# Kernel tuning notes

Measured on AMD Instinct MI355X. Metric: run time of the kernel, lower is better.

The kernel has to match this reference:

```python
import jax, jax.numpy as jnp
import numpy as np

B, S, E = 2, 2048, 2048
H = 16
KV_RANK = 512
ROPE = 64
NOPE = 64  # source sets qk_nope_dim = qk_rope_dim
VD = 128   # v_head_dim = head_dim
QD = ROPE + NOPE  # q_head_dim = 128


def setup_inputs() -> dict:
    key = jax.random.key(0)
    ks = jax.random.split(key, 5)
    sd = lambda fan_in: 1.0 / np.sqrt(fan_in)
    return {
        "x": jax.random.normal(ks[0], (B, S, E), jnp.float32),
        "attention_mask": jnp.zeros((1, 1, S, S), jnp.float32),
        "W_kv_down": jax.random.normal(ks[1], (KV_RANK + ROPE, E), jnp.float32) * sd(E),
        "W_kv_up": jax.random.normal(ks[2], (H * (VD + NOPE), KV_RANK), jnp.float32) * sd(KV_RANK),
        "W_q": jax.random.normal(ks[3], (H * QD, E), jnp.float32) * sd(E),
        "W_out": jax.random.normal(ks[4], (E, H * VD), jnp.float32) * sd(H * VD),
    }


def reference(x, attention_mask, W_kv_down, W_kv_up, W_q, W_out):
    scale = QD ** (-0.5)
    # down-project to latent + rope part
    compressed = jnp.einsum('bse,fe->bsf', x, W_kv_down)          # [B,S,KV_RANK+ROPE]
    kv_c, k_rope = compressed[..., :KV_RANK], compressed[..., KV_RANK:]
    # up-project latent to per-head v and k_nope
    kv_exp = jnp.einsum('bsr,fr->bsf', kv_c, W_kv_up)             # [B,S,H*(VD+NOPE)]
    kv_exp = kv_exp.reshape(B, S, H, VD + NOPE).transpose(0, 2, 1, 3)  # [B,H,S,VD+NOPE]
    v, k_nope = kv_exp[..., :VD], kv_exp[..., VD:]
    # shared rope key broadcast over heads, concat [rope, nope]
    k_rope_b = jnp.broadcast_to(k_rope[:, None], (B, H, S, ROPE))
    k = jnp.concatenate([k_rope_b, k_nope], axis=-1)              # [B,H,S,QD]
    # queries
    q = jnp.einsum('bse,fe->bsf', x, W_q).reshape(B, S, H, QD).transpose(0, 2, 1, 3)
    scores = jnp.einsum('bhsd,bhtd->bhst', q, k) * scale + attention_mask
    w = jax.nn.softmax(scores, axis=-1)
    out = jnp.einsum('bhst,bhtv->bhsv', w, v)                     # [B,H,S,VD]
    out = out.transpose(0, 2, 1, 3).reshape(B, S, H * VD)
    return jnp.einsum('bsf,ef->bse', out, W_out)
```

## Files before the change

kernel.cpp:

```cpp
#include <hip/hip_runtime.h>
#include <hip/hip_bf16.h>
#include <stdint.h>

typedef __bf16 bf16x8 __attribute__((ext_vector_type(8)));
typedef float f32x4 __attribute__((ext_vector_type(4)));
typedef float f32x16 __attribute__((ext_vector_type(16)));
typedef uint32_t u32x4 __attribute__((ext_vector_type(4)));
typedef unsigned short ushort_t;
typedef unsigned short ushort8v __attribute__((ext_vector_type(8)));

#define MFMA16 __builtin_amdgcn_mfma_f32_16x16x32_bf16
#define MFMA32 __builtin_amdgcn_mfma_f32_32x32x16_bf16

static constexpr int Bc = 2, Sc = 2048, Ec = 2048, Hc = 16;

__device__ __forceinline__ void gload16(const void* g, void* l) {
  __builtin_amdgcn_global_load_lds(
      (const __attribute__((address_space(1))) void*)g,
      (__attribute__((address_space(3))) void*)l, 16, 0, 0);
}

__device__ __forceinline__ ushort_t f2bf(float f) {
  uint32_t u = __float_as_uint(f);
  uint32_t r = (u + 0x7fffu + ((u >> 16) & 1u)) >> 16;
  return (ushort_t)r;
}
__device__ __forceinline__ float bf2f(ushort_t u) {
  return __uint_as_float((uint32_t)u << 16);
}
__device__ __forceinline__ uint32_t cvtpk(float a, float b) {
  uint32_t d;
  asm("v_cvt_pk_bf16_f32 %0, %1, %2" : "=v"(d) : "v"(a), "v"(b));
  return d;
}
__device__ __forceinline__ void plswap(uint32_t& a, uint32_t& b) {
  asm("v_permlane32_swap_b32 %0, %1" : "+v"(a), "+v"(b));
}

__global__ void cast_all(const float* __restrict__ x, const float* __restrict__ Wq,
                         const float* __restrict__ Wkvu, const float* __restrict__ Wout,
                         const float* __restrict__ Wkvd,
                         ushort_t* __restrict__ xb, ushort_t* __restrict__ wq,
                         ushort_t* __restrict__ wkvu, ushort_t* __restrict__ wout,
                         ushort_t* __restrict__ wkvd) {
  int i = blockIdx.x * 256 + threadIdx.x;
  const float* src;
  ushort_t* dst;
  int j;
  if (i < 2097152) { src = x; dst = xb; j = i; }
  else if (i < 3145728) { src = Wq; dst = wq; j = i - 2097152; }
  else if (i < 3538944) { src = Wkvu; dst = wkvu; j = i - 3145728; }
  else if (i < 4587520) { src = Wout; dst = wout; j = i - 3538944; }
  else {
    j = i - 4587520;
    int row = j >> 9, col4 = j & 511;
    ushort4 o;
    if (row < 576) {
      float4 v = ((const float4*)Wkvd)[row * 512 + col4];
      o.x = f2bf(v.x); o.y = f2bf(v.y); o.z = f2bf(v.z); o.w = f2bf(v.w);
    } else { o.x = 0; o.y = 0; o.z = 0; o.w = 0; }
    ((ushort4*)wkvd)[j] = o;
    return;
  }
  float4 v = ((const float4*)src)[j];
  ushort4 o;
  o.x = f2bf(v.x); o.y = f2bf(v.y); o.z = f2bf(v.z); o.w = f2bf(v.w);
  ((ushort4*)dst)[j] = o;
}

__global__ void mask_rearrange(const float* __restrict__ mask, ushort_t* __restrict__ m4) {
  const float INVLN2 = 1.4426950408889634f;
  int i = blockIdx.x * 256 + threadIdx.x;
  if (i >= 524288) return;
  int rr = i & 1, half = (i >> 1) & 1, kblk = (i >> 2) & 1, kt = (i >> 3) & 31, q = i >> 8;
  const float* src = mask + (size_t)q * 2048 + kt * 64 + kblk * 32 + half * 4 + rr * 16;
  float4 a = *(const float4*)src;
  float4 c = *(const float4*)(src + 8);
  ushort8v o;
  o[0] = f2bf(a.x * INVLN2); o[1] = f2bf(a.y * INVLN2);
  o[2] = f2bf(a.z * INVLN2); o[3] = f2bf(a.w * INVLN2);
  o[4] = f2bf(c.x * INVLN2); o[5] = f2bf(c.y * INVLN2);
  o[6] = f2bf(c.z * INVLN2); o[7] = f2bf(c.w * INVLN2);
  ((ushort8v*)m4)[i] = o;
}

template<int MODE>
__global__ __launch_bounds__(256, 2)
void gemm_bt(const ushort_t* __restrict__ A, int lda,
             const ushort_t* __restrict__ Bm, int ldb,
             void* __restrict__ Cout, int ldc,
             int M, int N, int K,
             char* __restrict__ vtb, char* __restrict__ kbuf)
{
  __shared__ __align__(16) ushort_t sA[2][128 * 32];
  __shared__ __align__(16) ushort_t sB[2][128 * 32];
  int tid = threadIdx.x;
  int nTn = N >> 7;
  int bid = blockIdx.x;
  int chunk = gridDim.x >> 3;
  bid = (bid & 7) * chunk + (bid >> 3);
  int tm = bid / nTn, tn = bid - tm * nTn;
  int wave = tid >> 6, lane = tid & 63;
  int wm = (wave >> 1) << 6, wn = (wave & 1) << 6;
  int l16 = lane & 15, g16 = lane >> 4;
  f32x4 acc[4][4] = {};
  int srow = tid >> 2, scol = (tid & 3) << 3;
  const ushort_t* Ag = A + (size_t)(tm * 128 + srow) * lda + scol;
  const ushort_t* Bg = Bm + (size_t)(tn * 128 + srow) * ldb + scol;
  ushort_t* sA0 = &sA[0][srow * 32 + scol];
  ushort_t* sA1 = &sA[1][srow * 32 + scol];
  ushort_t* sB0 = &sB[0][srow * 32 + scol];
  ushort_t* sB1 = &sB[1][srow * 32 + scol];
  for (int kt = 0; kt < K; kt += 64) {
    gload16(Ag, sA0);
    gload16(Ag + (size_t)64 * lda, sA0 + 64 * 32);
    gload16(Ag + 32, sA1);
    gload16(Ag + (size_t)64 * lda + 32, sA1 + 64 * 32);
    gload16(Bg, sB0);
    gload16(Bg + (size_t)64 * ldb, sB0 + 64 * 32);
    gload16(Bg + 32, sB1);
    gload16(Bg + (size_t)64 * ldb + 32, sB1 + 64 * 32);
    Ag += 64; Bg += 64;
    __syncthreads();
#pragma unroll
    for (int h2 = 0; h2 < 2; h2++) {
      bf16x8 af[4], bfr[4];
#pragma unroll
      for (int i = 0; i < 4; i++) af[i] = *(const bf16x8*)&sA[h2][(wm + i * 16 + l16) * 32 + g16 * 8];
#pragma unroll
      for (int i = 0; i < 4; i++) bfr[i] = *(const bf16x8*)&sB[h2][(wn + i * 16 + l16) * 32 + g16 * 8];
#pragma unroll
      for (int i = 0; i < 4; i++)
#pragma unroll
        for (int j = 0; j < 4; j++)
          acc[i][j] = MFMA16(af[i], bfr[j], acc[i][j], 0, 0, 0);
    }
    __syncthreads();
  }
#pragma unroll
  for (int i = 0; i < 4; i++) {
#pragma unroll
    for (int j = 0; j < 4; j++) {
      int grow0 = tm * 128 + wm + i * 16 + g16 * 4;
      int gcol = tn * 128 + wn + j * 16 + l16;
      if constexpr (MODE == 0) {
#pragma unroll
        for (int r = 0; r < 4; r++)
          ((ushort_t*)Cout)[(size_t)(grow0 + r) * ldc + gcol] = f2bf(acc[i][j][r]);
      } else if constexpr (MODE == 2) {
#pragma unroll
        for (int r = 0; r < 4; r++)
          ((float*)Cout)[(size_t)(grow0 + r) * ldc + gcol] = acc[i][j][r];
      } else {
        int h = gcol / 192, jj = gcol - h * 192;
        int b = grow0 >> 11, s0 = grow0 & 2047;
        size_t bh = (size_t)(b * Hc + h);
        if (jj < 128) {
          ushort4 pk;
          pk.x = f2bf(acc[i][j][0]); pk.y = f2bf(acc[i][j][1]);
          pk.z = f2bf(acc[i][j][2]); pk.w = f2bf(acc[i][j][3]);
          *(ushort4*)(vtb + bh * 524288 + (size_t)jj * 4096 + ((s0 >> 6) * 128) +
                      ((2 * (s0 & 63)) ^ ((jj & 7) << 4))) = pk;
        } else {
          int col = 64 + (jj - 128);
#pragma unroll
          for (int r = 0; r < 4; r++) {
            int s = s0 + r;
            *(ushort_t*)(kbuf + (bh * Sc + s) * 256 + ((2 * col) ^ ((s & 7) << 4))) = f2bf(acc[i][j][r]);
          }
        }
      }
    }
  }
}

__global__ void rope_fill(const ushort_t* __restrict__ comp, char* __restrict__ kbuf) {
  int i = blockIdx.x * 256 + threadIdx.x;
  if (i >= Bc * Sc * 8) return;
  int blk = i & 7;
  int m = i >> 3;
  int s = m & 2047, b = m >> 11;
  uint4 v = *(const uint4*)&comp[(size_t)m * 640 + 512 + blk * 8];
  int off = (blk * 16) ^ ((s & 7) << 4);
#pragma unroll
  for (int h = 0; h < Hc; h++) {
    *(uint4*)(kbuf + ((size_t)(b * Hc + h) * Sc + s) * 256 + off) = v;
  }
}

__global__ __launch_bounds__(128, 2)
void attn_kernel(const ushort_t* __restrict__ qb, const char* __restrict__ kbuf,
                 const char* __restrict__ vtb, const ushort_t* __restrict__ m4,
                 ushort_t* __restrict__ attn_o)
{
  __shared__ __align__(16) char smem[32768];
  char* sK = smem;
  char* sV = smem + 16384;
  const float scale2 = 0.12752081738040466f;
  int bid = blockIdx.x;
  bid = (bid & 7) * 128 + (bid >> 3);
  int qt = bid & 31, bh = bid >> 5;
  int b = bh >> 4, h = bh & 15;
  int tid = threadIdx.x, wave = tid >> 6, lane = tid & 63;
  int l32 = lane & 31, half = lane >> 5;
  int sx = (l32 & 7) << 4;
  int qbase = qt * 64 + wave * 32;

  bf16x8 qf[8];
  {
    const ushort_t* qp = qb + (size_t)(b * Sc + qbase + l32) * 2048 + h * 128 + half * 8;
#pragma unroll
    for (int ks = 0; ks < 8; ks++) qf[ks] = *(const bf16x8*)(qp + ks * 16);
  }

  float mrun = -3.0e38f, lrun = 0.f;
  f32x16 acco[4] = {};

  const char* kg = kbuf + (size_t)bh * 524288;
  const char* vg = vtb + (size_t)bh * 524288;
  const ushort8v* mq = (const ushort8v*)m4 + (size_t)(qbase + l32) * 256 + half * 2;

  for (int kt = 0; kt < 32; kt++) {
#pragma unroll
    for (int it = 0; it < 8; it++)
      gload16(kg + kt * 16384 + it * 2048 + tid * 16, sK + it * 2048 + tid * 16);
#pragma unroll
    for (int it = 0; it < 8; it++) {
      int l = it * 2048 + tid * 16;
      gload16(vg + (size_t)(l >> 7) * 4096 + kt * 128 + (l & 127), sV + l);
    }
    ushort8v mvv[4];
#pragma unroll
    for (int kb = 0; kb < 2; kb++)
#pragma unroll
      for (int rr = 0; rr < 2; rr++)
        mvv[kb * 2 + rr] = mq[kt * 8 + kb * 4 + rr];
    __syncthreads();

#pragma unroll
    for (int kblk = 0; kblk < 2; kblk++) {
      f32x16 sc = {};
      __builtin_amdgcn_s_setprio(1);
#pragma unroll
      for (int ks = 0; ks < 8; ks++) {
        bf16x8 kfr = *(const bf16x8*)(sK + (kblk * 32 + l32) * 256 +
                                      ((ks * 32 + half * 16) ^ sx));
        sc = MFMA32(kfr, qf[ks], sc, 0, 0, 0);
      }
      __builtin_amdgcn_s_setprio(0);

#pragma unroll
      for (int r = 0; r < 16; r++)
        sc[r] = sc[r] * scale2 + bf2f(mvv[kblk * 2 + (r >> 3)][r & 7]);
      float mx = sc[0];
#pragma unroll
      for (int r = 1; r < 16; r++) mx = fmaxf(mx, sc[r]);
      mx = fmaxf(mx, __shfl_xor(mx, 32));
      if (!__all(mx <= mrun + 11.0f)) {
        float mnew = fmaxf(mrun, mx);
        float corr = __builtin_amdgcn_exp2f(mrun - mnew);
        lrun *= corr; mrun = mnew;
#pragma unroll
        for (int r = 0; r < 16; r++) {
          float cr = __shfl(corr, (r & 3) + 8 * (r >> 2) + 4 * half);
#pragma unroll
          for (int vb = 0; vb < 4; vb++) acco[vb][r] *= cr;
        }
      }
      float rs = 0.f;
      uint32_t W[8];
#pragma unroll
      for (int m = 0; m < 4; m++) {
        float p0 = __builtin_amdgcn_exp2f(sc[4 * m + 0] - mrun);
        float p1 = __builtin_amdgcn_exp2f(sc[4 * m + 1] - mrun);
        float p2 = __builtin_amdgcn_exp2f(sc[4 * m + 2] - mrun);
        float p3 = __builtin_amdgcn_exp2f(sc[4 * m + 3] - mrun);
        rs += (p0 + p1) + (p2 + p3);
        W[2 * m] = cvtpk(p0, p1);
        W[2 * m + 1] = cvtpk(p2, p3);
      }
      lrun += rs;

      bf16x8 pf[2];
#pragma unroll
      for (int k2 = 0; k2 < 2; k2++) {
        uint32_t a0 = W[4 * k2 + 0], a1 = W[4 * k2 + 1];
        uint32_t b0 = W[4 * k2 + 2], b1 = W[4 * k2 + 3];
        plswap(a0, b0);
        plswap(a1, b1);
        u32x4 t; t[0] = a0; t[1] = a1; t[2] = b0; t[3] = b1;
        pf[k2] = __builtin_bit_cast(bf16x8, t);
      }

      __builtin_amdgcn_s_setprio(1);
#pragma unroll
      for (int k2 = 0; k2 < 2; k2++)
#pragma unroll
        for (int vb = 0; vb < 4; vb++) {
          bf16x8 vf = *(const bf16x8*)(sV + (vb * 32 + l32) * 128 +
                                       ((kblk * 64 + k2 * 32 + half * 16) ^ sx));
          acco[vb] = MFMA32(pf[k2], vf, acco[vb], 0, 0, 0);
        }
      __builtin_amdgcn_s_setprio(0);
    }

    __syncthreads();
  }

  lrun += __shfl_xor(lrun, 32);
#pragma unroll
  for (int r = 0; r < 16; r++) {
    int rowq = (r & 3) + 8 * (r >> 2) + 4 * half;
    float lr = __shfl(lrun, rowq);
    float inv = 1.0f / lr;
    int qrow = qbase + rowq;
    ushort_t* op = attn_o + (size_t)(b * Sc + qrow) * 2048 + h * 128 + l32;
#pragma unroll
    for (int vb = 0; vb < 4; vb++)
      op[vb * 32] = f2bf(acco[vb][r] * inv);
  }
}

extern "C" void kernel_launch(void* const* d_in, const int* in_sizes, int n_in,
                              void* d_out, int out_size, void* d_ws, size_t ws_size,
                              hipStream_t stream) {
  const float* x    = (const float*)d_in[0];
  const float* mask = (const float*)d_in[1];
  const float* Wkvd = (const float*)d_in[2];
  const float* Wkvu = (const float*)d_in[3];
  const float* Wq   = (const float*)d_in[4];
  const float* Wout = (const float*)d_in[5];

  char* ws = (char*)d_ws;
  size_t off = 0;
  auto alloc = [&](size_t bytes) { char* p = ws + off; off += (bytes + 255) & ~(size_t)255; return p; };
  ushort_t* xb   = (ushort_t*)alloc((size_t)4096 * 2048 * 2);
  ushort_t* wkvd = (ushort_t*)alloc((size_t)640 * 2048 * 2);
  ushort_t* wq   = (ushort_t*)alloc((size_t)2048 * 2048 * 2);
  ushort_t* wkvu = (ushort_t*)alloc((size_t)3072 * 512 * 2);
  ushort_t* wout = (ushort_t*)alloc((size_t)2048 * 2048 * 2);
  ushort_t* comp = (ushort_t*)alloc((size_t)4096 * 640 * 2);
  ushort_t* qbuf = (ushort_t*)alloc((size_t)4096 * 2048 * 2);
  char*     kbuf = alloc((size_t)Bc * Hc * Sc * 256);
  char*     vtb  = alloc((size_t)Bc * Hc * 524288);
  ushort_t* attn_o = xb;
  ushort_t* m4 = wq;

  cast_all<<<19200, 256, 0, stream>>>(x, Wq, Wkvu, Wout, Wkvd, xb, wq, wkvu, wout, wkvd);

  gemm_bt<0><<<32 * 5, 256, 0, stream>>>(xb, 2048, wkvd, 2048, comp, 640, 4096, 640, 2048, nullptr, nullptr);
  gemm_bt<0><<<32 * 16, 256, 0, stream>>>(xb, 2048, wq, 2048, qbuf, 2048, 4096, 2048, 2048, nullptr, nullptr);
  mask_rearrange<<<2048, 256, 0, stream>>>(mask, m4);
  gemm_bt<1><<<32 * 24, 256, 0, stream>>>(comp, 640, wkvu, 512, nullptr, 0, 4096, 3072, 512, vtb, kbuf);
  rope_fill<<<32768 / 256, 256, 0, stream>>>(comp, kbuf);
  attn_kernel<<<1024, 128, 0, stream>>>(qbuf, kbuf, vtb, m4, attn_o);
  gemm_bt<2><<<32 * 16, 256, 0, stream>>>(attn_o, 2048, wout, 2048, d_out, 2048, 4096, 2048, 2048, nullptr, nullptr);
}
```

Measured before the change: 263.0 us.

## Double-buffer GEMM LDS tiles and prefetch next K-slice during MFMA

Restructures the GEMM main loop to use two LDS buffers per K-half, issuing async global-to-LDS loads for the next K tile while computing on the current one, with vmcnt-based waits and raw barriers instead of full syncthreads. It also raises wave priority around the MFMA block. This aims to hide global load latency behind matrix math. In exchange it doubles LDS use to 64KB per block, which may reduce occupancy below the two blocks per CU the launch bounds request. The last iteration issues a redundant reload of tile zero.

```diff
diff --git a/kernel.cpp b/kernel.cpp
--- a/kernel.cpp
+++ b/kernel.cpp
@@ -92,8 +92,8 @@
              int M, int N, int K,
              char* __restrict__ vtb, char* __restrict__ kbuf)
 {
-  __shared__ __align__(16) ushort_t sA[2][128 * 32];
-  __shared__ __align__(16) ushort_t sB[2][128 * 32];
+  __shared__ __align__(16) ushort_t sA[2][2][128 * 32];
+  __shared__ __align__(16) ushort_t sB[2][2][128 * 32];
   int tid = threadIdx.x;
   int nTn = N >> 7;
   int bid = blockIdx.x;
@@ -107,36 +107,48 @@
   int srow = tid >> 2, scol = (tid & 3) << 3;
   const ushort_t* Ag = A + (size_t)(tm * 128 + srow) * lda + scol;
   const ushort_t* Bg = Bm + (size_t)(tn * 128 + srow) * ldb + scol;
-  ushort_t* sA0 = &sA[0][srow * 32 + scol];
-  ushort_t* sA1 = &sA[1][srow * 32 + scol];
-  ushort_t* sB0 = &sB[0][srow * 32 + scol];
-  ushort_t* sB1 = &sB[1][srow * 32 + scol];
-  for (int kt = 0; kt < K; kt += 64) {
-    gload16(Ag, sA0);
-    gload16(Ag + (size_t)64 * lda, sA0 + 64 * 32);
-    gload16(Ag + 32, sA1);
-    gload16(Ag + (size_t)64 * lda + 32, sA1 + 64 * 32);
-    gload16(Bg, sB0);
-    gload16(Bg + (size_t)64 * ldb, sB0 + 64 * 32);
-    gload16(Bg + 32, sB1);
-    gload16(Bg + (size_t)64 * ldb + 32, sB1 + 64 * 32);
-    Ag += 64; Bg += 64;
-    __syncthreads();
-#pragma unroll
-    for (int h2 = 0; h2 < 2; h2++) {
+  int Kt = K >> 6;
+
+  auto ISSUE = [&](int kk, int nb, int ks) {
+    const ushort_t* As = Ag + kk + ks * 32;
+    const ushort_t* Bs = Bg + kk + ks * 32;
+    ushort_t* dA = &sA[nb][ks][srow * 32 + scol];
+    ushort_t* dB = &sB[nb][ks][srow * 32 + scol];
+    gload16(As, dA);
+    gload16(As + (size_t)64 * lda, dA + 64 * 32);
+    gload16(Bs, dB);
+    gload16(Bs + (size_t)64 * ldb, dB + 64 * 32);
+  };
+
+  ISSUE(0, 0, 0);
+  ISSUE(0, 0, 1);
+  asm volatile("s_waitcnt vmcnt(4)" ::: "memory");
+  __builtin_amdgcn_s_barrier();
+
+  for (int kt = 0; kt < Kt; kt++) {
+    int buf = kt & 1;
+    int nb = (kt + 1) & 1;
+    int kkn = ((kt + 1) == Kt) ? 0 : (kt + 1) * 64;
+#pragma unroll
+    for (int ks = 0; ks < 2; ks++) {
+      ISSUE(kkn, nb, ks);
       bf16x8 af[4], bfr[4];
 #pragma unroll
-      for (int i = 0; i < 4; i++) af[i] = *(const bf16x8*)&sA[h2][(wm + i * 16 + l16) * 32 + g16 * 8];
-#pragma unroll
-      for (int i = 0; i < 4; i++) bfr[i] = *(const bf16x8*)&sB[h2][(wn + i * 16 + l16) * 32 + g16 * 8];
+      for (int i = 0; i < 4; i++) af[i] = *(const bf16x8*)&sA[buf][ks][(wm + i * 16 + l16) * 32 + g16 * 8];
+#pragma unroll
+      for (int i = 0; i < 4; i++) bfr[i] = *(const bf16x8*)&sB[buf][ks][(wn + i * 16 + l16) * 32 + g16 * 8];
+      __builtin_amdgcn_s_setprio(1);
 #pragma unroll
       for (int i = 0; i < 4; i++)
 #pragma unroll
         for (int j = 0; j < 4; j++)
           acc[i][j] = MFMA16(af[i], bfr[j], acc[i][j], 0, 0, 0);
+      __builtin_amdgcn_s_setprio(0);
+      asm volatile("s_waitcnt vmcnt(4)" ::: "memory");
+      __builtin_amdgcn_s_barrier();
     }
-    __syncthreads();
-  }
+  }
+
 #pragma unroll
   for (int i = 0; i < 4; i++) {
 #pragma unroll
```

After: 290.9 us. 10.6% more time.

## Software-pipeline K/V tile loads in attention and merge mask/rope prep kernels

Applied to the files above, without the earlier changes.

The attention inner loop is restructured so the next K tile is issued right after the QK MFMAs and the next V tile right after the PV MFMAs. Explicit vmcnt waits and barriers replace the full __syncthreads pair, so global-to-LDS copies overlap with the softmax and matmul work. Both 32-key sub-blocks are now computed together with a single max/rescale per 64-key tile, and the mask prefetch is double-buffered. Separately, the mask rearrange and rope fill kernels are merged into one launch to save a kernel launch. This relies on hand-counted vmcnt values and on single-buffered LDS reuse being correct, and it raises register pressure.

```diff
diff --git a/kernel.cpp b/kernel.cpp
--- a/kernel.cpp
+++ b/kernel.cpp
@@ -68,20 +68,34 @@
   ((ushort4*)dst)[j] = o;
 }
 
-__global__ void mask_rearrange(const float* __restrict__ mask, ushort_t* __restrict__ m4) {
+__global__ void prep_kernel(const float* __restrict__ mask, ushort_t* __restrict__ m4,
+                            const ushort_t* __restrict__ comp, char* __restrict__ kbuf) {
   const float INVLN2 = 1.4426950408889634f;
-  int i = blockIdx.x * 256 + threadIdx.x;
-  if (i >= 524288) return;
-  int rr = i & 1, half = (i >> 1) & 1, kblk = (i >> 2) & 1, kt = (i >> 3) & 31, q = i >> 8;
-  const float* src = mask + (size_t)q * 2048 + kt * 64 + kblk * 32 + half * 4 + rr * 16;
-  float4 a = *(const float4*)src;
-  float4 c = *(const float4*)(src + 8);
-  ushort8v o;
-  o[0] = f2bf(a.x * INVLN2); o[1] = f2bf(a.y * INVLN2);
-  o[2] = f2bf(a.z * INVLN2); o[3] = f2bf(a.w * INVLN2);
-  o[4] = f2bf(c.x * INVLN2); o[5] = f2bf(c.y * INVLN2);
-  o[6] = f2bf(c.z * INVLN2); o[7] = f2bf(c.w * INVLN2);
-  ((ushort8v*)m4)[i] = o;
+  int gb = blockIdx.x;
+  if (gb < 2048) {
+    int i = gb * 256 + threadIdx.x;
+    int rr = i & 1, half = (i >> 1) & 1, kblk = (i >> 2) & 1, kt = (i >> 3) & 31, q = i >> 8;
+    const float* src = mask + (size_t)q * 2048 + kt * 64 + kblk * 32 + half * 4 + rr * 16;
+    float4 a = *(const float4*)src;
+    float4 c = *(const float4*)(src + 8);
+    ushort8v o;
+    o[0] = f2bf(a.x * INVLN2); o[1] = f2bf(a.y * INVLN2);
+    o[2] = f2bf(a.z * INVLN2); o[3] = f2bf(a.w * INVLN2);
+    o[4] = f2bf(c.x * INVLN2); o[5] = f2bf(c.y * INVLN2);
+    o[6] = f2bf(c.z * INVLN2); o[7] = f2bf(c.w * INVLN2);
+    ((ushort8v*)m4)[i] = o;
+  } else {
+    int i = (gb - 2048) * 256 + threadIdx.x;
+    int blk = i & 7;
+    int m = i >> 3;
+    int s = m & 2047, b = m >> 11;
+    uint4 v = *(const uint4*)&comp[(size_t)m * 640 + 512 + blk * 8];
+    int off = (blk * 16) ^ ((s & 7) << 4);
+#pragma unroll
+    for (int h = 0; h < Hc; h++) {
+      *(uint4*)(kbuf + ((size_t)(b * Hc + h) * Sc + s) * 256 + off) = v;
+    }
+  }
 }
 
 template<int MODE>
@@ -174,20 +188,6 @@
   }
 }
 
-__global__ void rope_fill(const ushort_t* __restrict__ comp, char* __restrict__ kbuf) {
-  int i = blockIdx.x * 256 + threadIdx.x;
-  if (i >= Bc * Sc * 8) return;
-  int blk = i & 7;
-  int m = i >> 3;
-  int s = m & 2047, b = m >> 11;
-  uint4 v = *(const uint4*)&comp[(size_t)m * 640 + 512 + blk * 8];
-  int off = (blk * 16) ^ ((s & 7) << 4);
-#pragma unroll
-  for (int h = 0; h < Hc; h++) {
-    *(uint4*)(kbuf + ((size_t)(b * Hc + h) * Sc + s) * 256 + off) = v;
-  }
-}
-
 __global__ __launch_bounds__(128, 2)
 void attn_kernel(const ushort_t* __restrict__ qb, const char* __restrict__ kbuf,
                  const char* __restrict__ vtb, const ushort_t* __restrict__ m4,
@@ -220,91 +220,130 @@
   const char* vg = vtb + (size_t)bh * 524288;
   const ushort8v* mq = (const ushort8v*)m4 + (size_t)(qbase + l32) * 256 + half * 2;
 
-  for (int kt = 0; kt < 32; kt++) {
+  auto ISSUE_K = [&](int kt) {
 #pragma unroll
     for (int it = 0; it < 8; it++)
       gload16(kg + kt * 16384 + it * 2048 + tid * 16, sK + it * 2048 + tid * 16);
+  };
+  auto ISSUE_V = [&](int kt) {
 #pragma unroll
     for (int it = 0; it < 8; it++) {
       int l = it * 2048 + tid * 16;
       gload16(vg + (size_t)(l >> 7) * 4096 + kt * 128 + (l & 127), sV + l);
     }
-    ushort8v mvv[4];
-#pragma unroll
-    for (int kb = 0; kb < 2; kb++)
-#pragma unroll
-      for (int rr = 0; rr < 2; rr++)
-        mvv[kb * 2 + rr] = mq[kt * 8 + kb * 4 + rr];
-    __syncthreads();
-
-#pragma unroll
-    for (int kblk = 0; kblk < 2; kblk++) {
-      f32x16 sc = {};
-      __builtin_amdgcn_s_setprio(1);
-#pragma unroll
-      for (int ks = 0; ks < 8; ks++) {
-        bf16x8 kfr = *(const bf16x8*)(sK + (kblk * 32 + l32) * 256 +
-                                      ((ks * 32 + half * 16) ^ sx));
-        sc = MFMA32(kfr, qf[ks], sc, 0, 0, 0);
-      }
-      __builtin_amdgcn_s_setprio(0);
-
-#pragma unroll
-      for (int r = 0; r < 16; r++)
-        sc[r] = sc[r] * scale2 + bf2f(mvv[kblk * 2 + (r >> 3)][r & 7]);
-      float mx = sc[0];
-#pragma unroll
-      for (int r = 1; r < 16; r++) mx = fmaxf(mx, sc[r]);
-      mx = fmaxf(mx, __shfl_xor(mx, 32));
-      if (!__all(mx <= mrun + 11.0f)) {
-        float mnew = fmaxf(mrun, mx);
-        float corr = __builtin_amdgcn_exp2f(mrun - mnew);
-        lrun *= corr; mrun = mnew;
-#pragma unroll
-        for (int r = 0; r < 16; r++) {
-          float cr = __shfl(corr, (r & 3) + 8 * (r >> 2) + 4 * half);
-#pragma unroll
-          for (int vb = 0; vb < 4; vb++) acco[vb][r] *= cr;
-        }
-      }
-      float rs = 0.f;
-      uint32_t W[8];
-#pragma unroll
-      for (int m = 0; m < 4; m++) {
-        float p0 = __builtin_amdgcn_exp2f(sc[4 * m + 0] - mrun);
-        float p1 = __builtin_amdgcn_exp2f(sc[4 * m + 1] - mrun);
-        float p2 = __builtin_amdgcn_exp2f(sc[4 * m + 2] - mrun);
-        float p3 = __builtin_amdgcn_exp2f(sc[4 * m + 3] - mrun);
-        rs += (p0 + p1) + (p2 + p3);
-        W[2 * m] = cvtpk(p0, p1);
-        W[2 * m + 1] = cvtpk(p2, p3);
-      }
-      lrun += rs;
-
-      bf16x8 pf[2];
-#pragma unroll
-      for (int k2 = 0; k2 < 2; k2++) {
-        uint32_t a0 = W[4 * k2 + 0], a1 = W[4 * k2 + 1];
-        uint32_t b0 = W[4 * k2 + 2], b1 = W[4 * k2 + 3];
-        plswap(a0, b0);
-        plswap(a1, b1);
+  };
+
+  auto TILE = [&](int kt, ushort8v (&mc)[4], ushort8v (&mn)[4]) {
+    int ktn = (kt + 1) & 31;
+    asm volatile("s_waitcnt vmcnt(8)" ::: "memory");
+    __builtin_amdgcn_s_barrier();
+
+    f32x16 sc0 = {}, sc1 = {};
+    __builtin_amdgcn_s_setprio(1);
+#pragma unroll
+    for (int ks = 0; ks < 8; ks++) {
+      bf16x8 k0 = *(const bf16x8*)(sK + l32 * 256 + ((ks * 32 + half * 16) ^ sx));
+      bf16x8 k1 = *(const bf16x8*)(sK + (32 + l32) * 256 + ((ks * 32 + half * 16) ^ sx));
+      sc0 = MFMA32(k0, qf[ks], sc0, 0, 0, 0);
+      sc1 = MFMA32(k1, qf[ks], sc1, 0, 0, 0);
+    }
+    __builtin_amdgcn_s_setprio(0);
+    __builtin_amdgcn_s_barrier();
+
+    mn[0] = mq[ktn * 8 + 0]; mn[1] = mq[ktn * 8 + 1];
+    mn[2] = mq[ktn * 8 + 4]; mn[3] = mq[ktn * 8 + 5];
+    ISSUE_K(ktn);
+
+#pragma unroll
+    for (int r = 0; r < 16; r++) {
+      sc0[r] = sc0[r] * scale2 + bf2f(mc[r >> 3][r & 7]);
+      sc1[r] = sc1[r] * scale2 + bf2f(mc[2 + (r >> 3)][r & 7]);
+    }
+    float mx = fmaxf(sc0[0], sc1[0]);
+#pragma unroll
+    for (int r = 1; r < 16; r++) mx = fmaxf(mx, fmaxf(sc0[r], sc1[r]));
+    mx = fmaxf(mx, __shfl_xor(mx, 32));
+    if (!__all(mx <= mrun + 11.0f)) {
+      float mnew = fmaxf(mrun, mx);
+      float corr = __builtin_amdgcn_exp2f(mrun - mnew);
+      lrun *= corr; mrun = mnew;
+#pragma unroll
+      for (int r = 0; r < 16; r++) {
+        float cr = __shfl(corr, (r & 3) + 8 * (r >> 2) + 4 * half);
+#pragma unroll
+        for (int vb = 0; vb < 4; vb++) acco[vb][r] *= cr;
+      }
+    }
+    float rs = 0.f;
+    uint32_t W0[8], W1[8];
+#pragma unroll
+    for (int m = 0; m < 4; m++) {
+      float a0 = __builtin_amdgcn_exp2f(sc0[4 * m + 0] - mrun);
+      float a1 = __builtin_amdgcn_exp2f(sc0[4 * m + 1] - mrun);
+      float a2 = __builtin_amdgcn_exp2f(sc0[4 * m + 2] - mrun);
+      float a3 = __builtin_amdgcn_exp2f(sc0[4 * m + 3] - mrun);
+      float b0 = __builtin_amdgcn_exp2f(sc1[4 * m + 0] - mrun);
+      float b1 = __builtin_amdgcn_exp2f(sc1[4 * m + 1] - mrun);
+      float b2 = __builtin_amdgcn_exp2f(sc1[4 * m + 2] - mrun);
+      float b3 = __builtin_amdgcn_exp2f(sc1[4 * m + 3] - mrun);
+      rs += (a0 + a1) + (a2 + a3) + (b0 + b1) + (b2 + b3);
+      W0[2 * m] = cvtpk(a0, a1); W0[2 * m + 1] = cvtpk(a2, a3);
+      W1[2 * m] = cvtpk(b0, b1); W1[2 * m + 1] = cvtpk(b2, b3);
+    }
+    lrun += rs;
+
+    bf16x8 pf0[2], pf1[2];
+#pragma unroll
+    for (int k2 = 0; k2 < 2; k2++) {
+      {
+        uint32_t a0 = W0[4 * k2 + 0], a1 = W0[4 * k2 + 1];
+        uint32_t b0 = W0[4 * k2 + 2], b1 = W0[4 * k2 + 3];
+        plswap(a0, b0); plswap(a1, b1);
         u32x4 t; t[0] = a0; t[1] = a1; t[2] = b0; t[3] = b1;
-        pf[k2] = __builtin_bit_cast(bf16x8, t);
-      }
-
-      __builtin_amdgcn_s_setprio(1);
-#pragma unroll
-      for (int k2 = 0; k2 < 2; k2++)
-#pragma unroll
-        for (int vb = 0; vb < 4; vb++) {
-          bf16x8 vf = *(const bf16x8*)(sV + (vb * 32 + l32) * 128 +
-                                       ((kblk * 64 + k2 * 32 + half * 16) ^ sx));
-          acco[vb] = MFMA32(pf[k2], vf, acco[vb], 0, 0, 0);
-        }
-      __builtin_amdgcn_s_setprio(0);
-    }
-
-    __syncthreads();
+        pf0[k2] = __builtin_bit_cast(bf16x8, t);
+      }
+      {
+        uint32_t a0 = W1[4 * k2 + 0], a1 = W1[4 * k2 + 1];
+        uint32_t b0 = W1[4 * k2 + 2], b1 = W1[4 * k2 + 3];
+        plswap(a0, b0); plswap(a1, b1);
+        u32x4 t; t[0] = a0; t[1] = a1; t[2] = b0; t[3] = b1;
+        pf1[k2] = __builtin_bit_cast(bf16x8, t);
+      }
+    }
+
+    asm volatile("s_waitcnt vmcnt(12)" ::: "memory");
+    __builtin_amdgcn_s_barrier();
+
+    __builtin_amdgcn_s_setprio(1);
+#pragma unroll
+    for (int k2 = 0; k2 < 2; k2++) {
+#pragma unroll
+      for (int vb = 0; vb < 4; vb++) {
+        bf16x8 vf = *(const bf16x8*)(sV + (vb * 32 + l32) * 128 +
+                                     ((k2 * 32 + half * 16) ^ sx));
+        acco[vb] = MFMA32(pf0[k2], vf, acco[vb], 0, 0, 0);
+      }
+#pragma unroll
+      for (int vb = 0; vb < 4; vb++) {
+        bf16x8 vf = *(const bf16x8*)(sV + (vb * 32 + l32) * 128 +
+                                     ((64 + k2 * 32 + half * 16) ^ sx));
+        acco[vb] = MFMA32(pf1[k2], vf, acco[vb], 0, 0, 0);
+      }
+    }
+    __builtin_amdgcn_s_setprio(0);
+    __builtin_amdgcn_s_barrier();
+    ISSUE_V(ktn);
+  };
+
+  ushort8v mcA[4], mcB[4];
+  mcA[0] = mq[0]; mcA[1] = mq[1]; mcA[2] = mq[4]; mcA[3] = mq[5];
+  ISSUE_K(0);
+  ISSUE_V(0);
+
+#pragma unroll 1
+  for (int kt = 0; kt < 32; kt += 2) {
+    TILE(kt, mcA, mcB);
+    TILE(kt + 1, mcB, mcA);
   }
 
   lrun += __shfl_xor(lrun, 32);
@@ -350,9 +389,8 @@
 
   gemm_bt<0><<<32 * 5, 256, 0, stream>>>(xb, 2048, wkvd, 2048, comp, 640, 4096, 640, 2048, nullptr, nullptr);
   gemm_bt<0><<<32 * 16, 256, 0, stream>>>(xb, 2048, wq, 2048, qbuf, 2048, 4096, 2048, 2048, nullptr, nullptr);
-  mask_rearrange<<<2048, 256, 0, stream>>>(mask, m4);
+  prep_kernel<<<2176, 256, 0, stream>>>(mask, m4, comp, kbuf);
   gemm_bt<1><<<32 * 24, 256, 0, stream>>>(comp, 640, wkvu, 512, nullptr, 0, 4096, 3072, 512, vtb, kbuf);
-  rope_fill<<<32768 / 256, 256, 0, stream>>>(comp, kbuf);
   attn_kernel<<<1024, 128, 0, stream>>>(qbuf, kbuf, vtb, m4, attn_o);
   gemm_bt<2><<<32 * 16, 256, 0, stream>>>(attn_o, 2048, wout, 2048, d_out, 2048, 4096, 2048, 2048, nullptr, nullptr);
 }
```

Measured after the change: 264.6 us. No clear change (+0.6%).

## Load attention K/V fragments directly to registers via fragment-ordered layouts

Applied to the files above, without the earlier changes.

The attention kernel now runs as single-wave blocks that read K and V straight from global memory into MFMA-ready register fragments, with the next K block register-prefetched. This removes the LDS staging and the __syncthreads barriers. To make those loads coalesced, the KV up-projection epilogue, the rope fill and the mask rearrangement now write K, V^T and the mask in fragment order. The rope fill is also merged into the mask-prep kernel, saving a launch. In exchange, each wave re-reads K/V from global/L2 with no sharing between waves, and register pressure rises.

```diff
diff --git a/kernel.cpp b/kernel.cpp
--- a/kernel.cpp
+++ b/kernel.cpp
@@ -68,20 +68,37 @@
   ((ushort4*)dst)[j] = o;
 }
 
-__global__ void mask_rearrange(const float* __restrict__ mask, ushort_t* __restrict__ m4) {
+__global__ void prep_kernel(const float* __restrict__ mask, ushort_t* __restrict__ m4,
+                            const ushort_t* __restrict__ comp, char* __restrict__ kbuf) {
   const float INVLN2 = 1.4426950408889634f;
-  int i = blockIdx.x * 256 + threadIdx.x;
-  if (i >= 524288) return;
-  int rr = i & 1, half = (i >> 1) & 1, kblk = (i >> 2) & 1, kt = (i >> 3) & 31, q = i >> 8;
-  const float* src = mask + (size_t)q * 2048 + kt * 64 + kblk * 32 + half * 4 + rr * 16;
-  float4 a = *(const float4*)src;
-  float4 c = *(const float4*)(src + 8);
-  ushort8v o;
-  o[0] = f2bf(a.x * INVLN2); o[1] = f2bf(a.y * INVLN2);
-  o[2] = f2bf(a.z * INVLN2); o[3] = f2bf(a.w * INVLN2);
-  o[4] = f2bf(c.x * INVLN2); o[5] = f2bf(c.y * INVLN2);
-  o[6] = f2bf(c.z * INVLN2); o[7] = f2bf(c.w * INVLN2);
-  ((ushort8v*)m4)[i] = o;
+  int gb = blockIdx.x;
+  if (gb < 2048) {
+    int i = gb * 256 + threadIdx.x;
+    int rr = i & 1, half = (i >> 1) & 1, kblk = (i >> 2) & 1, kt = (i >> 3) & 31, q = i >> 8;
+    const float* src = mask + (size_t)q * 2048 + kt * 64 + kblk * 32 + half * 4 + rr * 16;
+    float4 a = *(const float4*)src;
+    float4 c = *(const float4*)(src + 8);
+    ushort8v o;
+    o[0] = f2bf(a.x * INVLN2); o[1] = f2bf(a.y * INVLN2);
+    o[2] = f2bf(a.z * INVLN2); o[3] = f2bf(a.w * INVLN2);
+    o[4] = f2bf(c.x * INVLN2); o[5] = f2bf(c.y * INVLN2);
+    o[6] = f2bf(c.z * INVLN2); o[7] = f2bf(c.w * INVLN2);
+    size_t u5 = ((((size_t)(q >> 5) * 32 + kt) * 4 + kblk * 2 + rr) * 64) + half * 32 + (q & 31);
+    ((ushort8v*)m4)[u5] = o;
+  } else {
+    int i = (gb - 2048) * 256 + threadIdx.x;
+    int blk = i & 7;
+    int m = i >> 3;
+    int s = m & 2047, b = m >> 11;
+    uint4 v = *(const uint4*)&comp[(size_t)m * 640 + 512 + blk * 8];
+    int kt = s >> 6, kblk = (s & 63) >> 5;
+    size_t base = (size_t)kt * 16384 + kblk * 8192 + (blk >> 1) * 1024 +
+                  ((blk & 1) * 32 + (s & 31)) * 16;
+#pragma unroll
+    for (int h = 0; h < Hc; h++) {
+      *(uint4*)(kbuf + (size_t)(b * Hc + h) * 524288 + base) = v;
+    }
+  }
 }
 
 template<int MODE>
@@ -155,56 +172,41 @@
         int h = gcol / 192, jj = gcol - h * 192;
         int b = grow0 >> 11, s0 = grow0 & 2047;
         size_t bh = (size_t)(b * Hc + h);
+        int kt = s0 >> 6, sl = s0 & 63;
+        int kblk = sl >> 5, l32s = sl & 31;
         if (jj < 128) {
+          int k2 = (sl >> 4) & 1, halfv = (sl >> 3) & 1, e0 = sl & 7;
           ushort4 pk;
           pk.x = f2bf(acc[i][j][0]); pk.y = f2bf(acc[i][j][1]);
           pk.z = f2bf(acc[i][j][2]); pk.w = f2bf(acc[i][j][3]);
-          *(ushort4*)(vtb + bh * 524288 + (size_t)jj * 4096 + ((s0 >> 6) * 128) +
-                      ((2 * (s0 & 63)) ^ ((jj & 7) << 4))) = pk;
+          *(ushort4*)(vtb + bh * 524288 + (size_t)kt * 16384 + kblk * 8192 + k2 * 4096 +
+                      (jj >> 5) * 1024 + (halfv * 32 + (jj & 31)) * 16 + e0 * 2) = pk;
         } else {
-          int col = 64 + (jj - 128);
-#pragma unroll
-          for (int r = 0; r < 4; r++) {
-            int s = s0 + r;
-            *(ushort_t*)(kbuf + (bh * Sc + s) * 256 + ((2 * col) ^ ((s & 7) << 4))) = f2bf(acc[i][j][r]);
-          }
+          int qd = jj - 64;
+          int ks = qd >> 4, halfq = (qd >> 3) & 1, e = qd & 7;
+          char* kp = kbuf + bh * 524288 + (size_t)kt * 16384 + kblk * 8192 + ks * 1024 +
+                     (halfq * 32 + l32s) * 16 + e * 2;
+#pragma unroll
+          for (int r = 0; r < 4; r++)
+            *(ushort_t*)(kp + r * 16) = f2bf(acc[i][j][r]);
         }
       }
     }
   }
 }
 
-__global__ void rope_fill(const ushort_t* __restrict__ comp, char* __restrict__ kbuf) {
-  int i = blockIdx.x * 256 + threadIdx.x;
-  if (i >= Bc * Sc * 8) return;
-  int blk = i & 7;
-  int m = i >> 3;
-  int s = m & 2047, b = m >> 11;
-  uint4 v = *(const uint4*)&comp[(size_t)m * 640 + 512 + blk * 8];
-  int off = (blk * 16) ^ ((s & 7) << 4);
-#pragma unroll
-  for (int h = 0; h < Hc; h++) {
-    *(uint4*)(kbuf + ((size_t)(b * Hc + h) * Sc + s) * 256 + off) = v;
-  }
-}
-
-__global__ __launch_bounds__(128, 2)
+__global__ __launch_bounds__(64, 2)
 void attn_kernel(const ushort_t* __restrict__ qb, const char* __restrict__ kbuf,
                  const char* __restrict__ vtb, const ushort_t* __restrict__ m4,
                  ushort_t* __restrict__ attn_o)
 {
-  __shared__ __align__(16) char smem[32768];
-  char* sK = smem;
-  char* sV = smem + 16384;
   const float scale2 = 0.12752081738040466f;
   int bid = blockIdx.x;
-  bid = (bid & 7) * 128 + (bid >> 3);
-  int qt = bid & 31, bh = bid >> 5;
+  bid = (bid & 7) * 256 + (bid >> 3);
+  int qt = bid & 63, bh = bid >> 6;
   int b = bh >> 4, h = bh & 15;
-  int tid = threadIdx.x, wave = tid >> 6, lane = tid & 63;
-  int l32 = lane & 31, half = lane >> 5;
-  int sx = (l32 & 7) << 4;
-  int qbase = qt * 64 + wave * 32;
+  int l = threadIdx.x, l32 = l & 31, half = l >> 5;
+  int qbase = qt * 32;
 
   bf16x8 qf[8];
   {
@@ -218,93 +220,95 @@
 
   const char* kg = kbuf + (size_t)bh * 524288;
   const char* vg = vtb + (size_t)bh * 524288;
-  const ushort8v* mq = (const ushort8v*)m4 + (size_t)(qbase + l32) * 256 + half * 2;
-
+  const ushort8v* mbase = (const ushort8v*)m4 + (size_t)qt * 8192;
+  int moff = half * 32 + l32;
+
+  bf16x8 kfA[8], kfB[8];
+  {
+    const char* p = kg + l * 16;
+#pragma unroll
+    for (int ks = 0; ks < 8; ks++) kfA[ks] = *(const bf16x8*)(p + ks * 1024);
+  }
+
+  auto PHASE = [&](int kt, int kblk, bf16x8 (&kfc)[8], bf16x8 (&kfn)[8],
+                   int ktn, int nkblk) {
+    bf16x8 vv[8];
+    {
+      const char* p = vg + (size_t)kt * 16384 + kblk * 8192 + l * 16;
+#pragma unroll
+      for (int i2 = 0; i2 < 8; i2++) vv[i2] = *(const bf16x8*)(p + i2 * 1024);
+    }
+    ushort8v mca = mbase[(kt * 4 + kblk * 2) * 64 + moff];
+    ushort8v mcb = mbase[(kt * 4 + kblk * 2 + 1) * 64 + moff];
+
+    f32x16 sc = {};
+    __builtin_amdgcn_s_setprio(1);
+#pragma unroll
+    for (int ks = 0; ks < 8; ks++) sc = MFMA32(kfc[ks], qf[ks], sc, 0, 0, 0);
+    __builtin_amdgcn_s_setprio(0);
+
+    {
+      const char* p = kg + (size_t)ktn * 16384 + nkblk * 8192 + l * 16;
+#pragma unroll
+      for (int ks = 0; ks < 8; ks++) kfn[ks] = *(const bf16x8*)(p + ks * 1024);
+    }
+
+#pragma unroll
+    for (int r = 0; r < 16; r++)
+      sc[r] = sc[r] * scale2 + bf2f((r < 8 ? mca : mcb)[r & 7]);
+    float mx = sc[0];
+#pragma unroll
+    for (int r = 1; r < 16; r++) mx = fmaxf(mx, sc[r]);
+    mx = fmaxf(mx, __shfl_xor(mx, 32));
+    if (!__all(mx <= mrun + 11.0f)) {
+      float mnew = fmaxf(mrun, mx);
+      float corr = __builtin_amdgcn_exp2f(mrun - mnew);
+      lrun *= corr; mrun = mnew;
+#pragma unroll
+      for (int r = 0; r < 16; r++) {
+        float cr = __shfl(corr, (r & 3) + 8 * (r >> 2) + 4 * half);
+#pragma unroll
+        for (int vb = 0; vb < 4; vb++) acco[vb][r] *= cr;
+      }
+    }
+    float rs = 0.f;
+    uint32_t W[8];
+#pragma unroll
+    for (int m = 0; m < 4; m++) {
+      float p0 = __builtin_amdgcn_exp2f(sc[4 * m + 0] - mrun);
+      float p1 = __builtin_amdgcn_exp2f(sc[4 * m + 1] - mrun);
+      float p2 = __builtin_amdgcn_exp2f(sc[4 * m + 2] - mrun);
+      float p3 = __builtin_amdgcn_exp2f(sc[4 * m + 3] - mrun);
+      rs += (p0 + p1) + (p2 + p3);
+      W[2 * m] = cvtpk(p0, p1);
+      W[2 * m + 1] = cvtpk(p2, p3);
+    }
+    lrun += rs;
+
+    bf16x8 pf[2];
+#pragma unroll
+    for (int k2 = 0; k2 < 2; k2++) {
+      uint32_t a0 = W[4 * k2 + 0], a1 = W[4 * k2 + 1];
+      uint32_t b0 = W[4 * k2 + 2], b1 = W[4 * k2 + 3];
+      plswap(a0, b0);
+      plswap(a1, b1);
+      u32x4 t; t[0] = a0; t[1] = a1; t[2] = b0; t[3] = b1;
+      pf[k2] = __builtin_bit_cast(bf16x8, t);
+    }
+
+    __builtin_amdgcn_s_setprio(1);
+#pragma unroll
+    for (int k2 = 0; k2 < 2; k2++)
+#pragma unroll
+      for (int vb = 0; vb < 4; vb++)
+        acco[vb] = MFMA32(pf[k2], vv[k2 * 4 + vb], acco[vb], 0, 0, 0);
+    __builtin_amdgcn_s_setprio(0);
+  };
+
+#pragma unroll 1
   for (int kt = 0; kt < 32; kt++) {
-#pragma unroll
-    for (int it = 0; it < 8; it++)
-      gload16(kg + kt * 16384 + it * 2048 + tid * 16, sK + it * 2048 + tid * 16);
-#pragma unroll
-    for (int it = 0; it < 8; it++) {
-      int l = it * 2048 + tid * 16;
-      gload16(vg + (size_t)(l >> 7) * 4096 + kt * 128 + (l & 127), sV + l);
-    }
-    ushort8v mvv[4];
-#pragma unroll
-    for (int kb = 0; kb < 2; kb++)
-#pragma unroll
-      for (int rr = 0; rr < 2; rr++)
-        mvv[kb * 2 + rr] = mq[kt * 8 + kb * 4 + rr];
-    __syncthreads();
-
-#pragma unroll
-    for (int kblk = 0; kblk < 2; kblk++) {
-      f32x16 sc = {};
-      __builtin_amdgcn_s_setprio(1);
-#pragma unroll
-      for (int ks = 0; ks < 8; ks++) {
-        bf16x8 kfr = *(const bf16x8*)(sK + (kblk * 32 + l32) * 256 +
-                                      ((ks * 32 + half * 16) ^ sx));
-        sc = MFMA32(kfr, qf[ks], sc, 0, 0, 0);
-      }
-      __builtin_amdgcn_s_setprio(0);
-
-#pragma unroll
-      for (int r = 0; r < 16; r++)
-        sc[r] = sc[r] * scale2 + bf2f(mvv[kblk * 2 + (r >> 3)][r & 7]);
-      float mx = sc[0];
-#pragma unroll
-      for (int r = 1; r < 16; r++) mx = fmaxf(mx, sc[r]);
-      mx = fmaxf(mx, __shfl_xor(mx, 32));
-      if (!__all(mx <= mrun + 11.0f)) {
-        float mnew = fmaxf(mrun, mx);
-        float corr = __builtin_amdgcn_exp2f(mrun - mnew);
-        lrun *= corr; mrun = mnew;
-#pragma unroll
-        for (int r = 0; r < 16; r++) {
-          float cr = __shfl(corr, (r & 3) + 8 * (r >> 2) + 4 * half);
-#pragma unroll
-          for (int vb = 0; vb < 4; vb++) acco[vb][r] *= cr;
-        }
-      }
-      float rs = 0.f;
-      uint32_t W[8];
-#pragma unroll
-      for (int m = 0; m < 4; m++) {
-        float p0 = __builtin_amdgcn_exp2f(sc[4 * m + 0] - mrun);
-        float p1 = __builtin_amdgcn_exp2f(sc[4 * m + 1] - mrun);
-        float p2 = __builtin_amdgcn_exp2f(sc[4 * m + 2] - mrun);
-        float p3 = __builtin_amdgcn_exp2f(sc[4 * m + 3] - mrun);
-        rs += (p0 + p1) + (p2 + p3);
-        W[2 * m] = cvtpk(p0, p1);
-        W[2 * m + 1] = cvtpk(p2, p3);
-      }
-      lrun += rs;
-
-      bf16x8 pf[2];
-#pragma unroll
-      for (int k2 = 0; k2 < 2; k2++) {
-        uint32_t a0 = W[4 * k2 + 0], a1 = W[4 * k2 + 1];
-        uint32_t b0 = W[4 * k2 + 2], b1 = W[4 * k2 + 3];
-        plswap(a0, b0);
-        plswap(a1, b1);
-        u32x4 t; t[0] = a0; t[1] = a1; t[2] = b0; t[3] = b1;
-        pf[k2] = __builtin_bit_cast(bf16x8, t);
-      }
-
-      __builtin_amdgcn_s_setprio(1);
-#pragma unroll
-      for (int k2 = 0; k2 < 2; k2++)
-#pragma unroll
-        for (int vb = 0; vb < 4; vb++) {
-          bf16x8 vf = *(const bf16x8*)(sV + (vb * 32 + l32) * 128 +
-                                       ((kblk * 64 + k2 * 32 + half * 16) ^ sx));
-          acco[vb] = MFMA32(pf[k2], vf, acco[vb], 0, 0, 0);
-        }
-      __builtin_amdgcn_s_setprio(0);
-    }
-
-    __syncthreads();
+    PHASE(kt, 0, kfA, kfB, kt, 1);
+    PHASE(kt, 1, kfB, kfA, (kt + 1) & 31, 0);
   }
 
   lrun += __shfl_xor(lrun, 32);
@@ -350,9 +354,8 @@
 
   gemm_bt<0><<<32 * 5, 256, 0, stream>>>(xb, 2048, wkvd, 2048, comp, 640, 4096, 640, 2048, nullptr, nullptr);
   gemm_bt<0><<<32 * 16, 256, 0, stream>>>(xb, 2048, wq, 2048, qbuf, 2048, 4096, 2048, 2048, nullptr, nullptr);
-  mask_rearrange<<<2048, 256, 0, stream>>>(mask, m4);
+  prep_kernel<<<2176, 256, 0, stream>>>(mask, m4, comp, kbuf);
   gemm_bt<1><<<32 * 24, 256, 0, stream>>>(comp, 640, wkvu, 512, nullptr, 0, 4096, 3072, 512, vtb, kbuf);
-  rope_fill<<<32768 / 256, 256, 0, stream>>>(comp, kbuf);
-  attn_kernel<<<1024, 128, 0, stream>>>(qbuf, kbuf, vtb, m4, attn_o);
+  attn_kernel<<<2048, 64, 0, stream>>>(qbuf, kbuf, vtb, m4, attn_o);
   gemm_bt<2><<<32 * 16, 256, 0, stream>>>(attn_o, 2048, wout, 2048, d_out, 2048, 4096, 2048, 2048, nullptr, nullptr);
 }
```

Result: no change. 267.3 us (+1.6%).
